# Kernel tuning notes

Hardware: AMD Instinct MI355X
Metric: run time of the kernel (lower is better)

Reference implementation:

```python
import jax, jax.numpy as jnp
import numpy as np

VOCAB = 32000
NUM_STATE = 256
NLABEL = 64
BATCH = 128
MAXLEN = 256
# transition init scale chosen so E[e^2]*S*a^2/3 ~= 1 -> per-step magnitude ~constant
TRANS_A = 0.208


def setup_inputs() -> dict:
    key = jax.random.key(0)
    k1, k2, k3, k4 = jax.random.split(key, 4)
    sentences = jax.random.randint(k1, (BATCH, MAXLEN), 0, VOCAB, dtype=jnp.int64)
    # original init: input.weight ~ U(0.5, 0.5) (constant 0.5). Use U(0.25, 0.75) so the
    # emission stays bounded away from 0 (it is divided by) while not being degenerate.
    emb = jax.random.uniform(k2, (VOCAB, NUM_STATE), minval=0.25, maxval=0.75, dtype=jnp.float32)
    transition = jax.random.uniform(k3, (NUM_STATE, NUM_STATE), minval=-TRANS_A, maxval=TRANS_A, dtype=jnp.float32)
    output = jax.random.uniform(k4, (NUM_STATE, NLABEL), minval=-0.5, maxval=0.5, dtype=jnp.float32)
    return {"sentences": sentences, "emb": emb, "transition": transition, "output": output}


def reference(sentences, emb, transition, output):
    # emission: [maxlen, batch, num_state]
    em = emb[sentences.T]

    def step_fwd(carry, e):  # carry: [B,S]
        nxt = jnp.einsum('ij,bj->bi', transition, carry) * e
        return nxt, nxt

    _, fw_rest = jax.lax.scan(step_fwd, em[0], em[1:])
    forwards = jnp.concatenate([em[:1], fw_rest], axis=0)  # [L,B,S]

    em_rev = em[::-1]

    def step_bwd(carry, e):  # uses transition^T
        nxt = jnp.einsum('ji,bj->bi', transition, carry) * e
        return nxt, nxt

    _, bw_rest = jax.lax.scan(step_bwd, em_rev[0], em_rev[1:])
    backwards = jnp.concatenate([em_rev[:1], bw_rest], axis=0)[::-1]  # time-aligned [L,B,S]

    expected_count = forwards * backwards / em
    score = jnp.einsum('lbs,sn->lbn', expected_count, output)
    return score.transpose(1, 0, 2)  # [batch, maxlen, nlabel]
```

## Files before the change

kernel.cpp:

```cpp
#include <hip/hip_runtime.h>
#include <hip/hip_bf16.h>


typedef _Float16 half8 __attribute__((ext_vector_type(8)));
typedef _Float16 half4 __attribute__((ext_vector_type(4)));
typedef float    f32x4 __attribute__((ext_vector_type(4)));
typedef unsigned long long u64;

#define LL 256
#define BB 128
#define SS 256
#define BT 16
#define RSTR8 67
#define RSTRO 65

static __device__ __forceinline__ f32x4 mfma16f(half8 a, half8 b, f32x4 c) {
  return __builtin_amdgcn_mfma_f32_16x16x32_f16(a, b, c, 0, 0, 0);
}

static __device__ __forceinline__ void lds_barrier() {
  __asm__ __volatile__("s_waitcnt lgkmcnt(0)\n\ts_barrier" ::: "memory");
}

static __device__ __forceinline__ u64 pack4(f32x4 v) {
  union { half4 h; u64 u; } x;
  x.h[0] = (_Float16)v[0];
  x.h[1] = (_Float16)v[1];
  x.h[2] = (_Float16)v[2];
  x.h[3] = (_Float16)v[3];
  return x.u;
}

static __device__ __forceinline__ half8 read_frag_s(const u64* plane, int row,
                                                    int kt, int q, int stride8) {
  const int o = row * stride8 + kt * 8 + q * 2;
  union { u64 u[2]; half8 v; } x;
  x.u[0] = plane[o];
  x.u[1] = plane[o + 1];
  return x.v;
}

__global__ __launch_bounds__(1024, 4)
void hmm_chain(const int* __restrict__ sent, const float* __restrict__ emb,
               const float* __restrict__ T, _Float16* __restrict__ fwh,
               _Float16* __restrict__ gh)
{
  __shared__ u64 s_carry[2][BT * RSTR8];
  __shared__ int s_tok[BT * 257];

  const int tid  = threadIdx.x;
  const int lane = tid & 63;
  const int w    = tid >> 6;
  const int m    = lane & 15;
  const int q    = lane >> 4;

  const int  bid = blockIdx.x;
  const bool fwd = (bid < 8);
  const int  bg0 = (fwd ? bid : bid - 8) * BT;
  _Float16* const obuf = fwd ? fwh : gh;
  const int  st  = 16 * w + 4 * q;

  for (int idx = tid; idx < BT * LL; idx += 1024) {
    int bb = idx >> 8, l2 = idx & 255;
    s_tok[bb * 257 + l2] = sent[(bg0 + bb) * LL + l2];
  }
  __syncthreads();

  half8 a_hi[8];
#pragma unroll
  for (int kt = 0; kt < 8; ++kt) {
    const int r0 = 16 * w + m;
    const int kb = 32 * kt + 8 * q;
    float v[8];
    if (fwd) {
      f32x4 f0 = *(const f32x4*)(T + r0 * 256 + kb);
      f32x4 f1 = *(const f32x4*)(T + r0 * 256 + kb + 4);
#pragma unroll
      for (int j = 0; j < 4; ++j) { v[j] = f0[j]; v[4 + j] = f1[j]; }
    } else {
#pragma unroll
      for (int j = 0; j < 8; ++j) v[j] = T[(kb + j) * 256 + r0];
    }
    half8 hi;
#pragma unroll
    for (int j = 0; j < 8; ++j) hi[j] = (_Float16)v[j];
    a_hi[kt] = hi;
  }

  const int l0 = fwd ? 0 : (LL - 1);
  {
    const int tok0 = s_tok[m * 257 + l0];
    f32x4 e0 = *(const f32x4*)(emb + (size_t)tok0 * 256 + st);
    u64 pc = pack4(e0);
    f32x4 one = 1.0f;
    u64 po = fwd ? pc : pack4(one);
    *(u64*)(obuf + (size_t)(l0 * BB + bg0 + m) * SS + st) = po;
    s_carry[0][m * RSTR8 + 4 * w + q] = pc;
  }

  f32x4 em_pref;
  {
    const int l1 = fwd ? 1 : (LL - 2);
    const int tok1 = s_tok[m * 257 + l1];
    em_pref = *(const f32x4*)(emb + (size_t)tok1 * 256 + st);
  }
  __syncthreads();

  for (int s = 1; s < LL; ++s) {
    const int l  = fwd ? s : (LL - 1) - s;
    const int rb = (s - 1) & 1, wb = s & 1;

    const u64* pr = &s_carry[rb][0];
    half8 bfr[8];
#pragma unroll
    for (int kt = 0; kt < 8; ++kt)
      bfr[kt] = read_frag_s(pr, m, kt, q, RSTR8);

    f32x4 em_now = em_pref;
    {
      const int ln = fwd ? (s + 1 < LL ? s + 1 : LL - 1)
                         : ((LL - 2) - s > 0 ? (LL - 2) - s : 0);
      const int tokn = s_tok[m * 257 + ln];
      em_pref = *(const f32x4*)(emb + (size_t)tokn * 256 + st);
    }

    f32x4 hh = 0.0f;
#pragma unroll
    for (int kt = 0; kt < 8; ++kt)
      hh = mfma16f(a_hi[kt], bfr[kt], hh);
    f32x4 v  = hh;
    f32x4 cn = v * em_now;

    u64 p0 = pack4(cn);
    s_carry[wb][m * RSTR8 + 4 * w + q] = p0;
    u64 sv = fwd ? p0 : pack4(v);
    *(u64*)(obuf + (size_t)(l * BB + bg0 + m) * SS + st) = sv;
    lds_barrier();
  }
}

__global__ __launch_bounds__(256, 2)
void hmm_score(const _Float16* __restrict__ fwh, const _Float16* __restrict__ gh,
               const float* __restrict__ outm, float* __restrict__ score)
{
  __shared__ u64 p_pl[64 * RSTR8];
  __shared__ u64 o_pl[64 * RSTRO];

  const int tid  = threadIdx.x;
  const int lane = tid & 63;
  const int w    = tid >> 6;
  const int rh   = w >> 1;
  const int np   = w & 1;
  const int m    = lane & 15;
  const int q    = lane >> 4;
  const int R0   = blockIdx.x * 64;

  {
    _Float16* o_h = (_Float16*)o_pl;
    for (int i = tid; i < 4096; i += 256) {
      f32x4 v = *(const f32x4*)(outm + i * 4);
      int k = i >> 4, n0 = (i & 15) * 4;
#pragma unroll
      for (int r = 0; r < 4; ++r)
        o_h[(n0 + r) * (RSTRO * 4) + k] = (_Float16)v[r];
    }
  }

  for (int idx = tid; idx < 64 * 64; idx += 256) {
    int row = idx >> 6, c = idx & 63;
    union { u64 u; half4 h; } a, b, p;
    a.u = *(const u64*)(fwh + (size_t)(R0 + row) * 256 + c * 4);
    b.u = *(const u64*)(gh  + (size_t)(R0 + row) * 256 + c * 4);
    p.h = a.h * b.h;
    p_pl[row * RSTR8 + c] = p.u;
  }
  lds_barrier();

  f32x4 acc[2][2];
#pragma unroll
  for (int j = 0; j < 2; ++j)
#pragma unroll
    for (int jn = 0; jn < 2; ++jn) acc[j][jn] = 0.0f;

#pragma unroll
  for (int kt = 0; kt < 8; ++kt) {
    half8 of[2];
#pragma unroll
    for (int jn = 0; jn < 2; ++jn)
      of[jn] = read_frag_s(o_pl, 16 * (2 * np + jn) + m, kt, q, RSTRO);
#pragma unroll
    for (int j = 0; j < 2; ++j) {
      half8 pf = read_frag_s(p_pl, 32 * rh + 16 * j + m, kt, q, RSTR8);
#pragma unroll
      for (int jn = 0; jn < 2; ++jn)
        acc[j][jn] = mfma16f(pf, of[jn], acc[j][jn]);
    }
  }

#pragma unroll
  for (int j = 0; j < 2; ++j) {
#pragma unroll
    for (int jn = 0; jn < 2; ++jn) {
#pragma unroll
      for (int r = 0; r < 4; ++r) {
        int row = R0 + 32 * rh + 16 * j + 4 * q + r;
        int l = row >> 7, b = row & 127;
        score[(size_t)b * 16384 + l * 64 + 16 * (2 * np + jn) + m] = acc[j][jn][r];
      }
    }
  }
}

extern "C" void kernel_launch(void* const* d_in, const int* in_sizes, int n_in,
                              void* d_out, int out_size, void* d_ws, size_t ws_size,
                              hipStream_t stream) {
  (void)in_sizes; (void)n_in; (void)out_size; (void)ws_size;
  const int*   sent = (const int*)d_in[0];
  const float* emb  = (const float*)d_in[1];
  const float* T    = (const float*)d_in[2];
  const float* outm = (const float*)d_in[3];
  _Float16* fwh = (_Float16*)d_ws;
  _Float16* gh  = fwh + (size_t)LL * BB * SS;

  hmm_chain<<<16, 1024, 0, stream>>>(sent, emb, T, fwh, gh);
  hmm_score<<<512, 256, 0, stream>>>(fwh, gh, outm, (float*)d_out);
}
```

Baseline: 294.8 us.

## Shrink chain blocks to 4 waves, each computing four 16-row output tiles

The sequential HMM chain kernel now runs 256 threads (4 waves) per block instead of 1024 (16 waves). Each wave holds four 16-row transition tiles in registers and issues 32 MFMAs per step instead of 8. Fewer waves per block make the per-step LDS barrier cheaper and let the four independent accumulators overlap MFMA latency. In exchange each wave carries more register pressure (32 half8 A fragments) and has a longer serial MFMA chain, and the carry fragments are still read once per wave.

```diff
diff --git a/kernel.cpp b/kernel.cpp
--- a/kernel.cpp
+++ b/kernel.cpp
@@ -40,7 +40,7 @@
   return x.v;
 }
 
-__global__ __launch_bounds__(1024, 4)
+__global__ __launch_bounds__(256, 1)
 void hmm_chain(const int* __restrict__ sent, const float* __restrict__ emb,
                const float* __restrict__ T, _Float16* __restrict__ fwh,
                _Float16* __restrict__ gh)
@@ -58,51 +58,60 @@
   const bool fwd = (bid < 8);
   const int  bg0 = (fwd ? bid : bid - 8) * BT;
   _Float16* const obuf = fwd ? fwh : gh;
-  const int  st  = 16 * w + 4 * q;
-
-  for (int idx = tid; idx < BT * LL; idx += 1024) {
+
+  for (int idx = tid; idx < BT * LL; idx += 256) {
     int bb = idx >> 8, l2 = idx & 255;
     s_tok[bb * 257 + l2] = sent[(bg0 + bb) * LL + l2];
   }
   __syncthreads();
 
-  half8 a_hi[8];
-#pragma unroll
-  for (int kt = 0; kt < 8; ++kt) {
-    const int r0 = 16 * w + m;
-    const int kb = 32 * kt + 8 * q;
-    float v[8];
-    if (fwd) {
-      f32x4 f0 = *(const f32x4*)(T + r0 * 256 + kb);
-      f32x4 f1 = *(const f32x4*)(T + r0 * 256 + kb + 4);
-#pragma unroll
-      for (int j = 0; j < 4; ++j) { v[j] = f0[j]; v[4 + j] = f1[j]; }
-    } else {
-#pragma unroll
-      for (int j = 0; j < 8; ++j) v[j] = T[(kb + j) * 256 + r0];
-    }
-    half8 hi;
-#pragma unroll
-    for (int j = 0; j < 8; ++j) hi[j] = (_Float16)v[j];
-    a_hi[kt] = hi;
+  half8 a_hi[4][8];
+#pragma unroll
+  for (int t = 0; t < 4; ++t) {
+    const int r0 = 64 * w + 16 * t + m;
+#pragma unroll
+    for (int kt = 0; kt < 8; ++kt) {
+      const int kb = 32 * kt + 8 * q;
+      float v[8];
+      if (fwd) {
+        f32x4 f0 = *(const f32x4*)(T + r0 * 256 + kb);
+        f32x4 f1 = *(const f32x4*)(T + r0 * 256 + kb + 4);
+#pragma unroll
+        for (int j = 0; j < 4; ++j) { v[j] = f0[j]; v[4 + j] = f1[j]; }
+      } else {
+#pragma unroll
+        for (int j = 0; j < 8; ++j) v[j] = T[(kb + j) * 256 + r0];
+      }
+      half8 hi;
+#pragma unroll
+      for (int j = 0; j < 8; ++j) hi[j] = (_Float16)v[j];
+      a_hi[t][kt] = hi;
+    }
   }
 
   const int l0 = fwd ? 0 : (LL - 1);
   {
     const int tok0 = s_tok[m * 257 + l0];
-    f32x4 e0 = *(const f32x4*)(emb + (size_t)tok0 * 256 + st);
-    u64 pc = pack4(e0);
     f32x4 one = 1.0f;
-    u64 po = fwd ? pc : pack4(one);
-    *(u64*)(obuf + (size_t)(l0 * BB + bg0 + m) * SS + st) = po;
-    s_carry[0][m * RSTR8 + 4 * w + q] = pc;
-  }
-
-  f32x4 em_pref;
+    const u64 pone = pack4(one);
+#pragma unroll
+    for (int t = 0; t < 4; ++t) {
+      const int st = 64 * w + 16 * t + 4 * q;
+      f32x4 e0 = *(const f32x4*)(emb + (size_t)tok0 * 256 + st);
+      u64 pc = pack4(e0);
+      u64 po = fwd ? pc : pone;
+      *(u64*)(obuf + (size_t)(l0 * BB + bg0 + m) * SS + st) = po;
+      s_carry[0][m * RSTR8 + 16 * w + 4 * t + q] = pc;
+    }
+  }
+
+  f32x4 em_pref[4];
   {
     const int l1 = fwd ? 1 : (LL - 2);
     const int tok1 = s_tok[m * 257 + l1];
-    em_pref = *(const f32x4*)(emb + (size_t)tok1 * 256 + st);
+#pragma unroll
+    for (int t = 0; t < 4; ++t)
+      em_pref[t] = *(const f32x4*)(emb + (size_t)tok1 * 256 + 64 * w + 16 * t + 4 * q);
   }
   __syncthreads();
 
@@ -116,25 +125,36 @@
     for (int kt = 0; kt < 8; ++kt)
       bfr[kt] = read_frag_s(pr, m, kt, q, RSTR8);
 
-    f32x4 em_now = em_pref;
+    f32x4 em_now[4];
+#pragma unroll
+    for (int t = 0; t < 4; ++t) em_now[t] = em_pref[t];
     {
       const int ln = fwd ? (s + 1 < LL ? s + 1 : LL - 1)
                          : ((LL - 2) - s > 0 ? (LL - 2) - s : 0);
       const int tokn = s_tok[m * 257 + ln];
-      em_pref = *(const f32x4*)(emb + (size_t)tokn * 256 + st);
-    }
-
-    f32x4 hh = 0.0f;
+#pragma unroll
+      for (int t = 0; t < 4; ++t)
+        em_pref[t] = *(const f32x4*)(emb + (size_t)tokn * 256 + 64 * w + 16 * t + 4 * q);
+    }
+
+    f32x4 acc[4];
+#pragma unroll
+    for (int t = 0; t < 4; ++t) acc[t] = 0.0f;
 #pragma unroll
     for (int kt = 0; kt < 8; ++kt)
-      hh = mfma16f(a_hi[kt], bfr[kt], hh);
-    f32x4 v  = hh;
-    f32x4 cn = v * em_now;
-
-    u64 p0 = pack4(cn);
-    s_carry[wb][m * RSTR8 + 4 * w + q] = p0;
-    u64 sv = fwd ? p0 : pack4(v);
-    *(u64*)(obuf + (size_t)(l * BB + bg0 + m) * SS + st) = sv;
+#pragma unroll
+      for (int t = 0; t < 4; ++t)
+        acc[t] = mfma16f(a_hi[t][kt], bfr[kt], acc[t]);
+
+#pragma unroll
+    for (int t = 0; t < 4; ++t) {
+      f32x4 cn = acc[t] * em_now[t];
+      u64 p0 = pack4(cn);
+      const int st = 64 * w + 16 * t + 4 * q;
+      s_carry[wb][m * RSTR8 + 16 * w + 4 * t + q] = p0;
+      u64 sv = fwd ? p0 : pack4(acc[t]);
+      *(u64*)(obuf + (size_t)(l * BB + bg0 + m) * SS + st) = sv;
+    }
     lds_barrier();
   }
 }
@@ -222,6 +242,6 @@
   _Float16* fwh = (_Float16*)d_ws;
   _Float16* gh  = fwh + (size_t)LL * BB * SS;
 
-  hmm_chain<<<16, 1024, 0, stream>>>(sent, emb, T, fwh, gh);
+  hmm_chain<<<16, 256, 0, stream>>>(sent, emb, T, fwh, gh);
   hmm_score<<<512, 256, 0, stream>>>(fwh, gh, outm, (float*)d_out);
 }
```

New measurement: 328.5 us. +11.4%, slower.

## Deepen emission prefetch, split MFMA chain, and move output store after barrier

Applied to the files above, without the earlier changes.

The serial recurrence loop is unrolled by three. Each step now prefetches emission rows three steps ahead through rotating registers, so the dependent global loads have more time to land. The eight-deep dependent MFMA accumulation is split into two independent four-deep chains that are summed at the end, which shortens the critical-path latency of each step. The global store of each step's output now comes after the LDS barrier, taking it off the path to the barrier. The costs are extra registers for the prefetched values and one extra vector add per step, and the unroll relies on the step count dividing evenly by three.

```diff
diff --git a/kernel.cpp b/kernel.cpp
--- a/kernel.cpp
+++ b/kernel.cpp
@@ -98,17 +98,21 @@
     s_carry[0][m * RSTR8 + 4 * w + q] = pc;
   }
 
-  f32x4 em_pref;
-  {
-    const int l1 = fwd ? 1 : (LL - 2);
-    const int tok1 = s_tok[m * 257 + l1];
-    em_pref = *(const f32x4*)(emb + (size_t)tok1 * 256 + st);
-  }
+  auto ldem = [&](int su) -> f32x4 {
+    su = su < LL ? su : LL - 1;
+    const int ln = fwd ? su : (LL - 1) - su;
+    const int tk = s_tok[m * 257 + ln];
+    return *(const f32x4*)(emb + (size_t)tk * 256 + st);
+  };
+
+  f32x4 emr0 = ldem(1);
+  f32x4 emr1 = ldem(2);
+  f32x4 emr2 = ldem(3);
   __syncthreads();
 
-  for (int s = 1; s < LL; ++s) {
-    const int l  = fwd ? s : (LL - 1) - s;
-    const int rb = (s - 1) & 1, wb = s & 1;
+  auto step = [&](int ss, f32x4& emr) {
+    const int l  = fwd ? ss : (LL - 1) - ss;
+    const int rb = (ss - 1) & 1, wb = ss & 1;
 
     const u64* pr = &s_carry[rb][0];
     half8 bfr[8];
@@ -116,26 +120,28 @@
     for (int kt = 0; kt < 8; ++kt)
       bfr[kt] = read_frag_s(pr, m, kt, q, RSTR8);
 
-    f32x4 em_now = em_pref;
-    {
-      const int ln = fwd ? (s + 1 < LL ? s + 1 : LL - 1)
-                         : ((LL - 2) - s > 0 ? (LL - 2) - s : 0);
-      const int tokn = s_tok[m * 257 + ln];
-      em_pref = *(const f32x4*)(emb + (size_t)tokn * 256 + st);
-    }
-
-    f32x4 hh = 0.0f;
-#pragma unroll
-    for (int kt = 0; kt < 8; ++kt)
-      hh = mfma16f(a_hi[kt], bfr[kt], hh);
-    f32x4 v  = hh;
+    f32x4 em_now = emr;
+    emr = ldem(ss + 3);
+
+    f32x4 aA = 0.0f, aB = 0.0f;
+#pragma unroll
+    for (int kt = 0; kt < 4; ++kt) aA = mfma16f(a_hi[kt], bfr[kt], aA);
+#pragma unroll
+    for (int kt = 4; kt < 8; ++kt) aB = mfma16f(a_hi[kt], bfr[kt], aB);
+    f32x4 v  = aA + aB;
     f32x4 cn = v * em_now;
 
     u64 p0 = pack4(cn);
     s_carry[wb][m * RSTR8 + 4 * w + q] = p0;
     u64 sv = fwd ? p0 : pack4(v);
+    lds_barrier();
     *(u64*)(obuf + (size_t)(l * BB + bg0 + m) * SS + st) = sv;
-    lds_barrier();
+  };
+
+  for (int s = 1; s < LL; s += 3) {
+    step(s + 0, emr0);
+    step(s + 1, emr1);
+    step(s + 2, emr2);
   }
 }
 
```

Measured after the change: 301.5 us. 2.3% more time.
